# Kernel tuning notes

Measured on AMD Instinct MI355X. Metric: run time of the kernel, lower is better.

The kernel has to match this reference:

```python
import jax, jax.numpy as jnp
import numpy as np
import math

D_MODEL, NHEAD, FACTOR = 1024, 16, 5
EPS = 1e-5


def layer_norm(x, g, b):
    m = jnp.mean(x, -1, keepdims=True)
    v = jnp.mean((x - m) ** 2, -1, keepdims=True)
    return (x - m) / jnp.sqrt(v + EPS) * g + b


def prob_attention(q, k, v, sample_key):
    # Informer ProbSparse causal self-attention. q,k,v: [B,H,L,E]
    B, H, L_Q, E = q.shape
    L_K = k.shape[2]
    U_part = min(FACTOR * int(np.ceil(np.log(L_K))), L_K)  # sampled keys per query
    u = min(FACTOR * int(np.ceil(np.log(L_Q))), L_Q)        # top queries kept
    idx = jax.random.randint(sample_key, (L_Q, U_part), 0, L_K)
    K_sample = k[:, :, idx, :]                               # [B,H,L_Q,U,E]
    QK_sample = jnp.einsum('bhle,bhlue->bhlu', q, K_sample)
    M = QK_sample.max(-1) - QK_sample.sum(-1) / L_K          # sparsity measure
    _, M_top = jax.lax.top_k(M, u)                           # [B,H,u] query indices
    Q_red = jnp.take_along_axis(q, M_top[..., None], axis=2) # [B,H,u,E]
    scores = jnp.einsum('bhue,bhse->bhus', Q_red, k) / math.sqrt(E)
    causal = jnp.arange(L_K)[None, None, None, :] > M_top[..., None]
    scores = jnp.where(causal, -1e9, scores)
    attn = jax.nn.softmax(scores, -1)
    upd = jnp.einsum('bhus,bhsd->bhud', attn, v)             # [B,H,u,E]
    ctx = jnp.cumsum(v, axis=2)                              # causal initial context
    b_i = jnp.arange(B)[:, None, None]
    h_i = jnp.arange(H)[None, :, None]
    return ctx.at[b_i, h_i, M_top].set(upd)


def full_attention(q, k, v):
    # q: [B,L,H,E], k,v: [B,S,H,E]; unmasked cross attention
    E = q.shape[-1]
    scores = jnp.einsum('blhe,bshe->bhls', q, k) / math.sqrt(E)
    A = jax.nn.softmax(scores, -1)
    return jnp.einsum('bhls,bshd->blhd', A, v)


def split_heads(t, B, L):
    return t.reshape(B, L, NHEAD, -1)


def decoder_layer(x, memory, sWq, sbq, sWk, sbk, sWv, sbv, sWo, sbo,
                  cWq, cbq, cWk, cbk, cWv, cbv, cWo, cbo,
                  W1, b1, W2, b2, g1, be1, g2, be2, g3, be3):
    B, L, D = x.shape
    S = memory.shape[1]
    # --- ProbSparse self-attention ---
    q = split_heads(x @ sWq + sbq, B, L).transpose(0, 2, 1, 3)
    k = split_heads(x @ sWk + sbk, B, L).transpose(0, 2, 1, 3)
    v = split_heads(x @ sWv + sbv, B, L).transpose(0, 2, 1, 3)
    ctx = prob_attention(q, k, v, jax.random.key(42))
    sa = ctx.transpose(0, 2, 1, 3).reshape(B, L, D) @ sWo + sbo
    x = layer_norm(x + sa, g1, be1)
    # --- full cross-attention ---
    q = split_heads(x @ cWq + cbq, B, L)
    k = split_heads(memory @ cWk + cbk, B, S)
    v = split_heads(memory @ cWv + cbv, B, S)
    ca = full_attention(q, k, v).reshape(B, L, D) @ cWo + cbo
    x = layer_norm(x + ca, g2, be2)
    # --- conv1d(k=1) FFN == pointwise MLP ---
    y = jax.nn.relu(x @ W1 + b1)
    y = y @ W2 + b2
    return layer_norm(x + y, g3, be3)


def setup_inputs() -> dict:
    key = jax.random.key(0)
    ks = jax.random.split(key, 32)
    D, F = D_MODEL, 4 * D_MODEL
    w = lambda k, sh: (jax.random.normal(k, sh, jnp.float32) * 0.02)
    inp = {
        'x': jax.random.normal(ks[0], (2, 2048, D), jnp.float32),
        'memory': jax.random.normal(ks[1], (2, 2048, D), jnp.float32),
    }
    names = ['sWq', 'sWk', 'sWv', 'sWo', 'cWq', 'cWk', 'cWv', 'cWo']
    for i, n in enumerate(names):
        inp[n] = w(ks[2 + i], (D, D))
        inp[n.replace('W', 'b')] = jnp.zeros((D,), jnp.float32)
    inp['W1'] = w(ks[10], (D, F)); inp['b1'] = jnp.zeros((F,), jnp.float32)
    inp['W2'] = w(ks[11], (F, D)); inp['b2'] = jnp.zeros((D,), jnp.float32)
    for i, n in enumerate(['1', '2', '3']):
        inp['g' + n] = jnp.ones((D,), jnp.float32)
        inp['be' + n] = jnp.zeros((D,), jnp.float32)
    return inp


def reference(x, memory, sWq, sbq, sWk, sbk, sWv, sbv, sWo, sbo,
              cWq, cbq, cWk, cbk, cWv, cbv, cWo, cbo,
              W1, b1, W2, b2, g1, be1, g2, be2, g3, be3):
    return decoder_layer(x, memory, sWq, sbq, sWk, sbk, sWv, sbv, sWo, sbo,
                         cWq, cbq, cWk, cbk, cWv, cbv, cWo, cbo,
                         W1, b1, W2, b2, g1, be1, g2, be2, g3, be3)
```

## Files before the change

### kernel.cpp

```cpp
#include <hip/hip_runtime.h>

static constexpr int BATCH  = 2;
static constexpr int SEQ    = 2048;
static constexpr int DMODEL = 1024;
static constexpr int NHEADS = 16;
static constexpr int EHEAD  = 64;
static constexpr int DFF    = 4096;
static constexpr int NTOP   = 40;

typedef unsigned short u16;
typedef __bf16 bf16x8_t __attribute__((ext_vector_type(8)));
typedef u16    u16x8_t  __attribute__((ext_vector_type(8)));
typedef u16    u16x4_t  __attribute__((ext_vector_type(4)));
typedef float  f32x4_t  __attribute__((ext_vector_type(4)));

static constexpr float QSCALE = 0.125f * 1.44269504088896f;
static constexpr float FIXM   = 12.0f;

static __device__ __forceinline__ u16 f2b(float f) {
  unsigned u = __builtin_bit_cast(unsigned, f);
  unsigned r = u + 0x7FFFu + ((u >> 16) & 1u);
  return (u16)(r >> 16);
}
static __device__ __forceinline__ u16 f2bf(float f) {
  __bf16 h = (__bf16)f;
  return __builtin_bit_cast(u16, h);
}
static __device__ __forceinline__ float b2f(u16 h) {
  unsigned u = ((unsigned)h) << 16;
  return __builtin_bit_cast(float, u);
}
static __device__ __forceinline__ f32x4_t mfma_bf16(u16x8_t a, u16x8_t b, f32x4_t c) {
  return __builtin_amdgcn_mfma_f32_16x16x32_bf16(
      __builtin_bit_cast(bf16x8_t, a), __builtin_bit_cast(bf16x8_t, b), c, 0, 0, 0);
}

#define GLD16(gsrc, ldst)                                                        \
  __builtin_amdgcn_global_load_lds(                                             \
      (const __attribute__((address_space(1))) void*)(gsrc),                    \
      (__attribute__((address_space(3))) void*)(ldst), 16, 0, 0)

static __device__ __forceinline__ void tf2x32(unsigned k0, unsigned k1,
                                              unsigned x0, unsigned x1,
                                              unsigned& o0, unsigned& o1) {
  unsigned ks2 = 0x1BD11BDAu ^ k0 ^ k1;
  x0 += k0; x1 += k1;
#define TFR(r) { x0 += x1; x1 = (x1 << r) | (x1 >> (32 - r)); x1 ^= x0; }
  TFR(13) TFR(15) TFR(26) TFR(6)  x0 += k1;  x1 += ks2 + 1u;
  TFR(17) TFR(29) TFR(16) TFR(24) x0 += ks2; x1 += k0 + 2u;
  TFR(13) TFR(15) TFR(26) TFR(6)  x0 += k0;  x1 += k1 + 3u;
  TFR(17) TFR(29) TFR(16) TFR(24) x0 += k1;  x1 += ks2 + 4u;
  TFR(13) TFR(15) TFR(26) TFR(6)  x0 += ks2; x1 += k0 + 5u;
#undef TFR
  o0 = x0; o1 = x1;
}

__global__ __launch_bounds__(256)
void prep_misc(const float* __restrict__ x, u16* __restrict__ xh,
               u16* __restrict__ xl, const float* __restrict__ mem,
               u16* __restrict__ memb, int* __restrict__ idx,
               const float* __restrict__ sbq, const float* __restrict__ sbk,
               float* __restrict__ biasqk, const float* __restrict__ cbk,
               const float* __restrict__ cbv, float* __restrict__ cbkv) {
  int blk = blockIdx.x, tid = threadIdx.x;
  if (blk < 4096) {
    int i = blk * 256 + tid;
    f32x4_t v = *(const f32x4_t*)(x + (size_t)i * 4);
    u16x4_t h, l;
#pragma unroll
    for (int d = 0; d < 4; ++d) {
      u16 hh = f2b(v[d]); h[d] = hh; l[d] = f2b(v[d] - b2f(hh));
    }
    *(u16x4_t*)(xh + (size_t)i * 4) = h;
    *(u16x4_t*)(xl + (size_t)i * 4) = l;
  } else if (blk < 8192) {
    int i = (blk - 4096) * 256 + tid;
    f32x4_t v = *(const f32x4_t*)(mem + (size_t)i * 4);
    u16x4_t o;
    o[0] = f2b(v[0]); o[1] = f2b(v[1]); o[2] = f2b(v[2]); o[3] = f2b(v[3]);
    *(u16x4_t*)(memb + (size_t)i * 4) = o;
  } else if (blk < 8512) {
    int i = (blk - 8192) * 256 + tid;
    unsigned c0, c1, o0, o1;
    tf2x32(0u, 42u, 0u, 1u, c0, c1);
    tf2x32(c0, c1, 0u, (unsigned)i, o0, o1);
    idx[i] = (int)((o0 ^ o1) & 2047u);
  } else {
    int i = (blk - 8512) * 256 + tid;
    if (i < 1024) biasqk[i] = sbq[i];
    else if (i < 2048) biasqk[i] = sbk[i - 1024];
    else if (i < 3072) cbkv[i - 2048] = cbk[i - 2048];
    else cbkv[i - 2048] = cbv[i - 3072];
  }
}

struct PrepW {
  const float* s2[2]; u16* dh2[2]; u16* dl2[2];
  const float* s6[6]; u16* d6[6];
  const float* W1; u16* W1T; const float* W2; u16* W2T;
};
__global__ __launch_bounds__(256)
void prep_weights(PrepW p) {
  __shared__ float t[64][65];
  int j = blockIdx.x;
  int c = threadIdx.x & 63, r4 = threadIdx.x >> 6;
  const float* in; u16* oh; u16* ol = nullptr;
  int K, N, k0, n0;
  if (j < 512) {
    int m = j >> 8, jj = j & 255;
    in = p.s2[m]; oh = p.dh2[m]; ol = p.dl2[m];
    K = 1024; N = 1024; n0 = (jj & 15) * 64; k0 = (jj >> 4) * 64;
  } else if (j < 2048) {
    int m = (j - 512) >> 8, jj = (j - 512) & 255;
    in = p.s6[m]; oh = p.d6[m];
    K = 1024; N = 1024; n0 = (jj & 15) * 64; k0 = (jj >> 4) * 64;
  } else if (j < 3072) {
    int jj = j - 2048;
    in = p.W1; oh = p.W1T;
    K = 1024; N = 4096; n0 = (jj & 63) * 64; k0 = (jj >> 6) * 64;
  } else {
    int jj = j - 3072;
    in = p.W2; oh = p.W2T;
    K = 4096; N = 1024; n0 = (jj & 15) * 64; k0 = (jj >> 4) * 64;
  }
#pragma unroll
  for (int i = 0; i < 16; ++i) {
    int r = r4 * 16 + i;
    t[r][c] = in[(size_t)(k0 + r) * N + n0 + c];
  }
  __syncthreads();
#pragma unroll
  for (int i = 0; i < 16; ++i) {
    int r = r4 * 16 + i;
    float f = t[c][r];
    u16 h = f2b(f);
    oh[(size_t)(n0 + r) * K + k0 + c] = h;
    if (ol) ol[(size_t)(n0 + r) * K + k0 + c] = f2b(f - b2f(h));
  }
}

template<int NF>
__global__ __launch_bounds__(256)
void gemm_bf(const u16* __restrict__ A, const u16* __restrict__ Bt,
             const float* __restrict__ bias, float* __restrict__ Cf,
             u16* __restrict__ Cb, int M, int N, int K, int relu) {
  __shared__ __align__(16) u16 sA[2][128 * 32];
  __shared__ __align__(16) u16 sB[2][NF * 32 * 32];
  const int tid = threadIdx.x;
  const int wave = tid >> 6, lane = tid & 63;
  const int m0 = blockIdx.x * 128, n0 = blockIdx.y * (NF * 32);
  const int wr = (wave >> 1) * 64, wc = (wave & 1) * (NF * 16);
  const int lr = lane & 15, kg = lane >> 4;
  const int wv = __builtin_amdgcn_readfirstlane(wave);

  int rowA[2], c8A[2];
#pragma unroll
  for (int rep = 0; rep < 2; ++rep) {
    int P = (rep * 256 + tid) << 4;
    int L = P ^ (((P >> 7) & 3) << 4);
    rowA[rep] = L >> 6; c8A[rep] = (L >> 4) & 3;
  }
  int rowB[NF / 2], c8B[NF / 2];
#pragma unroll
  for (int rep = 0; rep < NF / 2; ++rep) {
    int P = (rep * 256 + tid) << 4;
    int L = P ^ (((P >> 7) & 3) << 4);
    rowB[rep] = L >> 6; c8B[rep] = (L >> 4) & 3;
  }

  f32x4_t acc[4][NF];
#pragma unroll
  for (int i = 0; i < 4; ++i)
#pragma unroll
    for (int j = 0; j < NF; ++j) acc[i][j] = f32x4_t{0.f, 0.f, 0.f, 0.f};

  auto STAGE = [&](int buf, int k0) {
#pragma unroll
    for (int rep = 0; rep < 2; ++rep)
      GLD16(A + (size_t)(m0 + rowA[rep]) * K + k0 + c8A[rep] * 8,
            &sA[buf][(rep * 256 + wv * 64) * 8]);
#pragma unroll
    for (int rep = 0; rep < NF / 2; ++rep)
      GLD16(Bt + (size_t)(n0 + rowB[rep]) * K + k0 + c8B[rep] * 8,
            &sB[buf][(rep * 256 + wv * 64) * 8]);
  };

  const int nk = K >> 5;
  STAGE(0, 0);
  __syncthreads();
  for (int t = 0; t < nk; ++t) {
    const int cur = t & 1;
    if (t + 1 < nk) STAGE(cur ^ 1, (t + 1) << 5);
    u16x8_t a8[4], b8[NF];
#pragma unroll
    for (int mi = 0; mi < 4; ++mi) {
      int La = (wr + mi * 16 + lr) * 64 + kg * 16;
      a8[mi] = *(const u16x8_t*)((const char*)sA[cur] + (La ^ (((La >> 7) & 3) << 4)));
    }
#pragma unroll
    for (int ni = 0; ni < NF; ++ni) {
      int Lb = (wc + ni * 16 + lr) * 64 + kg * 16;
      b8[ni] = *(const u16x8_t*)((const char*)sB[cur] + (Lb ^ (((Lb >> 7) & 3) << 4)));
    }
#pragma unroll
    for (int mi = 0; mi < 4; ++mi)
#pragma unroll
      for (int ni = 0; ni < NF; ++ni)
        acc[mi][ni] = mfma_bf16(a8[mi], b8[ni], acc[mi][ni]);
    __syncthreads();
  }
#pragma unroll
  for (int ni = 0; ni < NF; ++ni) {
    int col = n0 + wc + ni * 16 + lr;
    float bc = bias[col];
#pragma unroll
    for (int mi = 0; mi < 4; ++mi)
#pragma unroll
      for (int r = 0; r < 4; ++r) {
        int row = m0 + wr + mi * 16 + kg * 4 + r;
        float vv = acc[mi][ni][r] + bc;
        if (relu) vv = fmaxf(vv, 0.f);
        if (Cf) Cf[(size_t)row * N + col] = vv;
        if (Cb) Cb[(size_t)row * N + col] = f2b(vv);
      }
  }
}

template<int NF>
__global__ __launch_bounds__(256)
void gemm_ks(const u16* __restrict__ A, const u16* __restrict__ Bt,
             const float* __restrict__ bias, float* __restrict__ C0,
             float* __restrict__ C1, int M, int N, int K) {
  __shared__ __align__(16) u16 sA[2][128 * 32];
  __shared__ __align__(16) u16 sB[2][NF * 32 * 32];
  const int tid = threadIdx.x;
  const int wave = tid >> 6, lane = tid & 63;
  const int m0 = blockIdx.x * 128, n0 = blockIdx.y * (NF * 32);
  const int zz = blockIdx.z;
  const int Kh = K >> 1;
  const u16* Ab = A + (size_t)zz * Kh;
  const u16* Bb = Bt + (size_t)zz * Kh;
  float* Cf = zz ? C1 : C0;
  const int wr = (wave >> 1) * 64, wc = (wave & 1) * (NF * 16);
  const int lr = lane & 15, kg = lane >> 4;
  const int wv = __builtin_amdgcn_readfirstlane(wave);

  int rowA[2], c8A[2];
#pragma unroll
  for (int rep = 0; rep < 2; ++rep) {
    int P = (rep * 256 + tid) << 4;
    int L = P ^ (((P >> 7) & 3) << 4);
    rowA[rep] = L >> 6; c8A[rep] = (L >> 4) & 3;
  }
  int rowB[NF / 2], c8B[NF / 2];
#pragma unroll
  for (int rep = 0; rep < NF / 2; ++rep) {
    int P = (rep * 256 + tid) << 4;
    int L = P ^ (((P >> 7) & 3) << 4);
    rowB[rep] = L >> 6; c8B[rep] = (L >> 4) & 3;
  }

  f32x4_t acc[4][NF];
#pragma unroll
  for (int i = 0; i < 4; ++i)
#pragma unroll
    for (int j = 0; j < NF; ++j) acc[i][j] = f32x4_t{0.f, 0.f, 0.f, 0.f};

  auto STAGE = [&](int buf, int k0) {
#pragma unroll
    for (int rep = 0; rep < 2; ++rep)
      GLD16(Ab + (size_t)(m0 + rowA[rep]) * K + k0 + c8A[rep] * 8,
            &sA[buf][(rep * 256 + wv * 64) * 8]);
#pragma unroll
    for (int rep = 0; rep < NF / 2; ++rep)
      GLD16(Bb + (size_t)(n0 + rowB[rep]) * K + k0 + c8B[rep] * 8,
            &sB[buf][(rep * 256 + wv * 64) * 8]);
  };

  const int nk = Kh >> 5;
  STAGE(0, 0);
  __syncthreads();
  for (int t = 0; t < nk; ++t) {
    const int cur = t & 1;
    if (t + 1 < nk) STAGE(cur ^ 1, (t + 1) << 5);
    u16x8_t a8[4], b8[NF];
#pragma unroll
    for (int mi = 0; mi < 4; ++mi) {
      int La = (wr + mi * 16 + lr) * 64 + kg * 16;
      a8[mi] = *(const u16x8_t*)((const char*)sA[cur] + (La ^ (((La >> 7) & 3) << 4)));
    }
#pragma unroll
    for (int ni = 0; ni < NF; ++ni) {
      int Lb = (wc + ni * 16 + lr) * 64 + kg * 16;
      b8[ni] = *(const u16x8_t*)((const char*)sB[cur] + (Lb ^ (((Lb >> 7) & 3) << 4)));
    }
#pragma unroll
    for (int mi = 0; mi < 4; ++mi)
#pragma unroll
      for (int ni = 0; ni < NF; ++ni)
        acc[mi][ni] = mfma_bf16(a8[mi], b8[ni], acc[mi][ni]);
    __syncthreads();
  }
#pragma unroll
  for (int ni = 0; ni < NF; ++ni) {
    int col = n0 + wc + ni * 16 + lr;
    float bc = (zz == 0) ? bias[col] : 0.f;
#pragma unroll
    for (int mi = 0; mi < 4; ++mi)
#pragma unroll
      for (int r = 0; r < 4; ++r) {
        int row = m0 + wr + mi * 16 + kg * 4 + r;
        Cf[(size_t)row * N + col] = acc[mi][ni][r] + bc;
      }
  }
}

template<int NF>
__global__ __launch_bounds__(256)
void gemm4_bf(const u16* __restrict__ Ah, const u16* __restrict__ Al,
              const u16* __restrict__ Bh, const u16* __restrict__ Bl,
              const float* __restrict__ bias, float* __restrict__ Cf,
              int M, int N, int K) {
  __shared__ __align__(16) u16 sAh[2][128 * 32];
  __shared__ __align__(16) u16 sAl[2][128 * 32];
  __shared__ __align__(16) u16 sBh[2][NF * 32 * 32];
  __shared__ __align__(16) u16 sBl[2][NF * 32 * 32];
  const int tid = threadIdx.x;
  const int wave = tid >> 6, lane = tid & 63;
  const int m0 = blockIdx.x * 128, n0 = blockIdx.y * (NF * 32);
  const int wr = (wave >> 1) * 64, wc = (wave & 1) * (NF * 16);
  const int lr = lane & 15, kg = lane >> 4;
  const int wv = __builtin_amdgcn_readfirstlane(wave);

  int rowA[2], c8A[2];
#pragma unroll
  for (int rep = 0; rep < 2; ++rep) {
    int P = (rep * 256 + tid) << 4;
    int L = P ^ (((P >> 7) & 3) << 4);
    rowA[rep] = L >> 6; c8A[rep] = (L >> 4) & 3;
  }
  int rowB[NF / 2], c8B[NF / 2];
#pragma unroll
  for (int rep = 0; rep < NF / 2; ++rep) {
    int P = (rep * 256 + tid) << 4;
    int L = P ^ (((P >> 7) & 3) << 4);
    rowB[rep] = L >> 6; c8B[rep] = (L >> 4) & 3;
  }

  f32x4_t acc[4][NF];
#pragma unroll
  for (int i = 0; i < 4; ++i)
#pragma unroll
    for (int j = 0; j < NF; ++j) acc[i][j] = f32x4_t{0.f, 0.f, 0.f, 0.f};

  auto STAGE = [&](int buf, int k0) {
#pragma unroll
    for (int rep = 0; rep < 2; ++rep) {
      GLD16(Ah + (size_t)(m0 + rowA[rep]) * K + k0 + c8A[rep] * 8,
            &sAh[buf][(rep * 256 + wv * 64) * 8]);
      GLD16(Al + (size_t)(m0 + rowA[rep]) * K + k0 + c8A[rep] * 8,
            &sAl[buf][(rep * 256 + wv * 64) * 8]);
    }
#pragma unroll
    for (int rep = 0; rep < NF / 2; ++rep) {
      GLD16(Bh + (size_t)(n0 + rowB[rep]) * K + k0 + c8B[rep] * 8,
            &sBh[buf][(rep * 256 + wv * 64) * 8]);
      GLD16(Bl + (size_t)(n0 + rowB[rep]) * K + k0 + c8B[rep] * 8,
            &sBl[buf][(rep * 256 + wv * 64) * 8]);
    }
  };

  const int nk = K >> 5;
  STAGE(0, 0);
  __syncthreads();
  for (int t = 0; t < nk; ++t) {
    const int cur = t & 1;
    if (t + 1 < nk) STAGE(cur ^ 1, (t + 1) << 5);
    u16x8_t ah[4], al[4], bh[NF], bl[NF];
#pragma unroll
    for (int mi = 0; mi < 4; ++mi) {
      int La = (wr + mi * 16 + lr) * 64 + kg * 16;
      int off = La ^ (((La >> 7) & 3) << 4);
      ah[mi] = *(const u16x8_t*)((const char*)sAh[cur] + off);
      al[mi] = *(const u16x8_t*)((const char*)sAl[cur] + off);
    }
#pragma unroll
    for (int ni = 0; ni < NF; ++ni) {
      int Lb = (wc + ni * 16 + lr) * 64 + kg * 16;
      int off = Lb ^ (((Lb >> 7) & 3) << 4);
      bh[ni] = *(const u16x8_t*)((const char*)sBh[cur] + off);
      bl[ni] = *(const u16x8_t*)((const char*)sBl[cur] + off);
    }
#pragma unroll
    for (int mi = 0; mi < 4; ++mi)
#pragma unroll
      for (int ni = 0; ni < NF; ++ni) {
        acc[mi][ni] = mfma_bf16(ah[mi], bh[ni], acc[mi][ni]);
        acc[mi][ni] = mfma_bf16(ah[mi], bl[ni], acc[mi][ni]);
        acc[mi][ni] = mfma_bf16(al[mi], bh[ni], acc[mi][ni]);
      }
    __syncthreads();
  }
#pragma unroll
  for (int ni = 0; ni < NF; ++ni) {
    int col = n0 + wc + ni * 16 + lr;
    float bc = bias[col];
#pragma unroll
    for (int mi = 0; mi < 4; ++mi)
#pragma unroll
      for (int r = 0; r < 4; ++r) {
        int row = m0 + wr + mi * 16 + kg * 4 + r;
        Cf[(size_t)row * N + col] = acc[mi][ni][r] + bc;
      }
  }
}

__global__ __launch_bounds__(256)
void probM_kernel(const float* __restrict__ qk, const int* __restrict__ idx,
                  float* __restrict__ Mv) {
  int blk = blockIdx.x;
  int xcd = blk & 7, j = blk >> 3;
  int b = xcd >> 2;
  int part = (xcd & 3) * 128 + j;
  int l = part * 4 + (threadIdx.x >> 6);
  int lane = threadIdx.x & 63;
  const float* qrow = qk + ((size_t)b * SEQ + l) * 2048 + lane * 16;
  f32x4_t qv0 = *(const f32x4_t*)(qrow);
  f32x4_t qv1 = *(const f32x4_t*)(qrow + 4);
  f32x4_t qv2 = *(const f32x4_t*)(qrow + 8);
  f32x4_t qv3 = *(const f32x4_t*)(qrow + 12);
  const int* ip = idx + l * NTOP;
  const float* kbase = qk + (size_t)b * SEQ * 2048 + 1024 + lane * 16;
  float mmax = -3.0e38f, msum = 0.f;
  for (int pass = 0; pass < 4; ++pass) {
    int lo = pass << 9;
#pragma unroll 4
    for (int u = 0; u < NTOP; ++u) {
      int ki = ip[u];
      if ((unsigned)(ki - lo) < 512u) {
        const float* kr = kbase + (size_t)ki * 2048;
        f32x4_t k0 = *(const f32x4_t*)(kr);
        f32x4_t k1 = *(const f32x4_t*)(kr + 4);
        f32x4_t k2 = *(const f32x4_t*)(kr + 8);
        f32x4_t k3 = *(const f32x4_t*)(kr + 12);
        float p = qv0[0] * k0[0] + qv0[1] * k0[1] + qv0[2] * k0[2] + qv0[3] * k0[3]
                + qv1[0] * k1[0] + qv1[1] * k1[1] + qv1[2] * k1[2] + qv1[3] * k1[3]
                + qv2[0] * k2[0] + qv2[1] * k2[1] + qv2[2] * k2[2] + qv2[3] * k2[3]
                + qv3[0] * k3[0] + qv3[1] * k3[1] + qv3[2] * k3[2] + qv3[3] * k3[3];
        p += __shfl_xor(p, 1);
        p += __shfl_xor(p, 2);
        mmax = fmaxf(mmax, p);
        msum += p;
      }
    }
  }
  if ((lane & 3) == 0) {
    int hh = lane >> 2;
    Mv[((size_t)b * NHEADS + hh) * SEQ + l] = mmax - msum * (1.f / 2048.f);
  }
}

__global__ __launch_bounds__(256)
void topk_kernel(const float* __restrict__ Mv, int* __restrict__ Mtop) {
  int bh = blockIdx.x;
  int tid = threadIdx.x;
  int lane = tid & 63, wv = tid >> 6;
  float v8[8];
#pragma unroll
  for (int j = 0; j < 8; ++j) v8[j] = Mv[bh * 2048 + j * 256 + tid];
  __shared__ float wrv[4];
  __shared__ int wri[4];
  __shared__ int winner;
  for (int it = 0; it < NTOP; ++it) {
    float best = v8[0];
    int bj = 0;
#pragma unroll
    for (int j = 1; j < 8; ++j)
      if (v8[j] > best) { best = v8[j]; bj = j; }
    int bi = bj * 256 + tid;
#pragma unroll
    for (int m = 1; m < 64; m <<= 1) {
      float ov = __shfl_xor(best, m);
      int oi = __shfl_xor(bi, m);
      if (ov > best || (ov == best && oi < bi)) { best = ov; bi = oi; }
    }
    if (lane == 0) { wrv[wv] = best; wri[wv] = bi; }
    __syncthreads();
    if (tid == 0) {
      float bv = wrv[0]; int bbi = wri[0];
#pragma unroll
      for (int t = 1; t < 4; ++t)
        if (wrv[t] > bv || (wrv[t] == bv && wri[t] < bbi)) { bv = wrv[t]; bbi = wri[t]; }
      Mtop[bh * NTOP + it] = bbi;
      winner = bbi;
    }
    __syncthreads();
    int w = winner;
#pragma unroll
    for (int j = 0; j < 8; ++j)
      if ((w >> 8) == j && (w & 255) == tid) v8[j] = -3.4e38f;
  }
}

__global__ __launch_bounds__(256)
void kvpack_self(const float* __restrict__ qk, const u16* __restrict__ vbf,
                 u16* __restrict__ kpack, u16* __restrict__ vpack) {
  int bh = blockIdx.x, ch = blockIdx.y;
  int b = bh >> 4, hh = bh & 15;
  int tid = threadIdx.x;
  __shared__ u16 vt[64][80];
#pragma unroll
  for (int rep = 0; rep < 2; ++rep) {
    int u = rep * 256 + tid;
    int key = u >> 3, c = u & 7;
    const float* ksrc = qk + ((size_t)(b * SEQ + ch * 64 + key)) * 2048 + 1024 + hh * 64 + c * 8;
    f32x4_t k0 = *(const f32x4_t*)ksrc;
    f32x4_t k1 = *(const f32x4_t*)(ksrc + 4);
    u16x8_t d;
    d[0] = f2bf(k0[0]); d[1] = f2bf(k0[1]); d[2] = f2bf(k0[2]); d[3] = f2bf(k0[3]);
    d[4] = f2bf(k1[0]); d[5] = f2bf(k1[1]); d[6] = f2bf(k1[2]); d[7] = f2bf(k1[3]);
    int slot = (key & 3) | (((key >> 3) & 1) << 2);
    *(u16x8_t*)(kpack + ((size_t)bh * SEQ + ch * 64 + key) * 64 + ((c ^ slot) * 8)) = d;
    u16x8_t dv = *(const u16x8_t*)(vbf + ((size_t)(b * SEQ + ch * 64 + key)) * 1024 + hh * 64 + c * 8);
    *(u16x8_t*)(&vt[key][c * 8]) = dv;
  }
  __syncthreads();
#pragma unroll
  for (int rep = 0; rep < 2; ++rep) {
    int u = rep * 256 + tid;
    int e = u >> 3, c = u & 7;
    int kb = (c ^ (e & 7)) * 8;
    u16x8_t d;
#pragma unroll
    for (int j = 0; j < 8; ++j) d[j] = vt[kb + j][e];
    *(u16x8_t*)(vpack + (((size_t)bh * 32 + ch) * 64 + e) * 64 + c * 8) = d;
  }
}

__global__ __launch_bounds__(256)
void probAttn_kernel(const float* __restrict__ qk, const u16* __restrict__ kpack,
                     const u16* __restrict__ vpack, const int* __restrict__ Mtop,
                     float* __restrict__ Opart, float* __restrict__ ml) {
  const int bh = blockIdx.x, b = bh >> 4, hh = bh & 15;
  const int split = blockIdx.y;
  const int tid = threadIdx.x, wave = tid >> 6, lane = tid & 63;
  const int lr = lane & 15, kg = lane >> 4;
  const int wv = __builtin_amdgcn_readfirstlane(wave);
  __shared__ __align__(16) u16 Qs[48 * 64];
  __shared__ __align__(16) u16 Kt[2][64 * 64];
  __shared__ __align__(16) u16 Vt[2][64 * 64];

#pragma unroll
  for (int rep = 0; rep < 3; ++rep) {
    int j = tid + 256 * rep;
    int row = j >> 4, c4 = j & 15;
    int qi = Mtop[bh * NTOP + (row < NTOP ? row : NTOP - 1)];
    f32x4_t v4 = *(const f32x4_t*)(qk + ((size_t)b * SEQ + qi) * 2048 + hh * EHEAD + c4 * 4);
    u16x4_t b4;
    b4[0] = f2bf(v4[0] * QSCALE); b4[1] = f2bf(v4[1] * QSCALE);
    b4[2] = f2bf(v4[2] * QSCALE); b4[3] = f2bf(v4[3] * QSCALE);
    *(u16x4_t*)((char*)Qs + ((row * 128 + c4 * 8) ^ ((row & 7) << 4))) = b4;
  }

  const int qtile = (wave < 3) ? wave : 2;
  const int qrow_g = qtile * 16 + lr;
  const int iq = (qrow_g < NTOP) ? Mtop[bh * NTOP + qrow_g] : -1;

  int koffs[2][4], voffs[2][4], kbase16[4];
#pragma unroll
  for (int t4 = 0; t4 < 4; ++t4) {
    int arow = ((t4 >> 1) << 5) + ((lr >> 2) << 3) + ((t4 & 1) << 2) + (lr & 3);
    int slot = (arow & 3) | (((arow >> 3) & 1) << 2);
#pragma unroll
    for (int ks = 0; ks < 2; ++ks)
      koffs[ks][t4] = ((arow << 7) + (ks << 6) + (kg << 4)) ^ (slot << 4);
    kbase16[t4] = ((t4 >> 1) << 5) + (kg << 3) + ((t4 & 1) << 2);
  }
#pragma unroll
  for (int ne = 0; ne < 4; ++ne) {
    int e = ne * 16 + lr;
#pragma unroll
    for (int ks2 = 0; ks2 < 2; ++ks2)
      voffs[ks2][ne] = ((e << 7) + (ks2 << 6) + (kg << 4)) ^ ((e & 7) << 4);
  }
  const int maskbase = split * 256 - iq;

  const char* kgl = (const char*)kpack + (size_t)bh * SEQ * 128 + (size_t)split * 4 * 8192;
  const char* vgl = (const char*)vpack + (size_t)bh * 32 * 8192 + (size_t)split * 4 * 8192;
  auto STAGE = [&](int buf, int t) {
    GLD16(kgl + (size_t)t * 8192 + wv * 2048 + lane * 16, (char*)Kt[buf] + wv * 2048);
    GLD16(kgl + (size_t)t * 8192 + wv * 2048 + 1024 + lane * 16, (char*)Kt[buf] + wv * 2048 + 1024);
    GLD16(vgl + (size_t)t * 8192 + wv * 2048 + lane * 16, (char*)Vt[buf] + wv * 2048);
    GLD16(vgl + (size_t)t * 8192 + wv * 2048 + 1024 + lane * 16, (char*)Vt[buf] + wv * 2048 + 1024);
  };

  STAGE(0, 0);
  __syncthreads();

  u16x8_t bq[2];
  {
    int qrow = qtile * 16 + lr;
#pragma unroll
    for (int ks = 0; ks < 2; ++ks)
      bq[ks] = *(u16x8_t*)((char*)Qs + ((qrow * 128 + ks * 64 + kg * 16) ^ ((qrow & 7) << 4)));
  }

  f32x4_t oacc[4];
#pragma unroll
  for (int i = 0; i < 4; ++i) oacc[i] = f32x4_t{0.f, 0.f, 0.f, 0.f};
  float lsum = 0.f;

  for (int t = 0; t < 4; ++t) {
    const int cur = t & 1;
    if (t + 1 < 4) STAGE(cur ^ 1, t + 1);
    const char* kb = (const char*)Kt + cur * 8192;
    const char* vb = (const char*)Vt + cur * 8192;
    f32x4_t s[4];
#pragma unroll
    for (int i = 0; i < 4; ++i) s[i] = f32x4_t{-FIXM, -FIXM, -FIXM, -FIXM};
#pragma unroll
    for (int ks = 0; ks < 2; ++ks)
#pragma unroll
      for (int t4 = 0; t4 < 4; ++t4) {
        u16x8_t ak = *(const u16x8_t*)(kb + koffs[ks][t4]);
        s[t4] = mfma_bf16(ak, bq[ks], s[t4]);
      }
    const int mb = t * 64 + maskbase;
#pragma unroll
    for (int t4 = 0; t4 < 4; ++t4)
#pragma unroll
      for (int r = 0; r < 4; ++r)
        if (mb + kbase16[t4] + r > 0) s[t4][r] = -1e9f;
#pragma unroll
    for (int t4 = 0; t4 < 4; ++t4)
#pragma unroll
      for (int r = 0; r < 4; ++r) {
        float p = exp2f(s[t4][r]);
        s[t4][r] = p; lsum += p;
      }
#pragma unroll
    for (int ks2 = 0; ks2 < 2; ++ks2) {
      u16x8_t pa;
#pragma unroll
      for (int j = 0; j < 4; ++j) {
        pa[j] = f2bf(s[2 * ks2][j]);
        pa[4 + j] = f2bf(s[2 * ks2 + 1][j]);
      }
#pragma unroll
      for (int ne = 0; ne < 4; ++ne) {
        u16x8_t bv = *(const u16x8_t*)(vb + voffs[ks2][ne]);
        oacc[ne] = mfma_bf16(pa, bv, oacc[ne]);
      }
    }
    __syncthreads();
  }

  lsum += __shfl_xor(lsum, 16);
  lsum += __shfl_xor(lsum, 32);

  if (wave < 3) {
    float* ob = Opart + (((size_t)(bh * 8 + split)) * 48 + qtile * 16) * 64;
#pragma unroll
    for (int ne = 0; ne < 4; ++ne)
#pragma unroll
      for (int r = 0; r < 4; ++r)
        ob[(size_t)(kg * 4 + r) * 64 + ne * 16 + lr] = oacc[ne][r];
    if (kg == 0)
      ml[((size_t)(bh * 8 + split)) * 48 + qtile * 16 + lr] = lsum;
  }
}

__global__ __launch_bounds__(64)
void probCombine_kernel(const float* __restrict__ Opart, const float* __restrict__ ml,
                        const int* __restrict__ Mtop, u16* __restrict__ ctxb) {
  int bh = blockIdx.x / NTOP, q = blockIdx.x % NTOP;
  int e = threadIdx.x;
  int b = bh >> 4, hh = bh & 15;
  float lstar = 0.f, acc = 0.f;
#pragma unroll
  for (int s = 0; s < 8; ++s) {
    lstar += ml[((size_t)(bh * 8 + s)) * 48 + q];
    acc += Opart[(((size_t)(bh * 8 + s)) * 48 + q) * 64 + e];
  }
  int row = Mtop[bh * NTOP + q];
  ctxb[((size_t)b * SEQ + row) * DMODEL + hh * EHEAD + e] = f2bf(acc / lstar);
}

__global__ __launch_bounds__(64)
void scanA_kernel(const u16* __restrict__ v, float* __restrict__ csum) {
  int bh = blockIdx.x, ch = blockIdx.y;
  int b = bh >> 4, hh = bh & 15, e = threadIdx.x;
  size_t base = ((size_t)b * SEQ + ch * 128) * DMODEL + hh * EHEAD + e;
  float run = 0.f;
  for (int i = 0; i < 128; ++i) run += b2f(v[base + (size_t)i * DMODEL]);
  csum[(bh * 16 + ch) * 64 + e] = run;
}
__global__ __launch_bounds__(64)
void scanB_kernel(const u16* __restrict__ v, const float* __restrict__ csum,
                  u16* __restrict__ ctxb) {
  int bh = blockIdx.x, ch = blockIdx.y;
  int b = bh >> 4, hh = bh & 15, e = threadIdx.x;
  float run = 0.f;
  for (int cc = 0; cc < ch; ++cc) run += csum[(bh * 16 + cc) * 64 + e];
  size_t base = ((size_t)b * SEQ + ch * 128) * DMODEL + hh * EHEAD + e;
  for (int i = 0; i < 128; ++i) {
    run += b2f(v[base + (size_t)i * DMODEL]);
    ctxb[base + (size_t)i * DMODEL] = f2bf(run);
  }
}

__global__ __launch_bounds__(256)
void kvpack_kernel(const u16* __restrict__ kv, u16* __restrict__ kpack,
                   u16* __restrict__ vpack) {
  int bh = blockIdx.x, ch = blockIdx.y;
  int b = bh >> 4, hh = bh & 15;
  int tid = threadIdx.x;
  __shared__ u16 vt[64][80];
#pragma unroll
  for (int rep = 0; rep < 2; ++rep) {
    int u = rep * 256 + tid;
    int key = u >> 3, c = u & 7;
    u16x8_t d = *(const u16x8_t*)(kv + ((size_t)(b * SEQ + ch * 64 + key)) * 2048 + hh * 64 + c * 8);
    int slot = (key & 3) | (((key >> 3) & 1) << 2);
    *(u16x8_t*)(kpack + ((size_t)bh * SEQ + ch * 64 + key) * 64 + ((c ^ slot) * 8)) = d;
    u16x8_t dv = *(const u16x8_t*)(kv + ((size_t)(b * SEQ + ch * 64 + key)) * 2048 + 1024 + hh * 64 + c * 8);
    *(u16x8_t*)(&vt[key][c * 8]) = dv;
  }
  __syncthreads();
#pragma unroll
  for (int rep = 0; rep < 2; ++rep) {
    int u = rep * 256 + tid;
    int e = u >> 3, c = u & 7;
    int kb = (c ^ (e & 7)) * 8;
    u16x8_t d;
#pragma unroll
    for (int j = 0; j < 8; ++j) d[j] = vt[kb + j][e];
    *(u16x8_t*)(vpack + (((size_t)bh * 32 + ch) * 64 + e) * 64 + c * 8) = d;
  }
}

__global__ __launch_bounds__(512)
void cross_attn_kernel(const float* __restrict__ q2, const u16* __restrict__ kpack,
                       const u16* __restrict__ vpack, u16* __restrict__ cab) {
  const int bh = blockIdx.x, b = bh >> 4, hh = bh & 15;
  const int qt0 = blockIdx.y * 128;
  const int tid = threadIdx.x, wave = tid >> 6, lane = tid & 63;
  const int lr = lane & 15, kg = lane >> 4;
  const int wv = __builtin_amdgcn_readfirstlane(wave);
  __shared__ __align__(16) u16 Qs[128 * 64];
  __shared__ __align__(16) u16 Kt[2][64 * 64];
  __shared__ __align__(16) u16 Vt[2][64 * 64];

#pragma unroll
  for (int i = 0; i < 4; ++i) {
    int j = tid + 512 * i;
    int row = j >> 4, c4 = j & 15;
    f32x4_t v4 = *(const f32x4_t*)(q2 + ((size_t)b * SEQ + qt0 + row) * DMODEL + hh * EHEAD + c4 * 4);
    u16x4_t b4;
    b4[0] = f2bf(v4[0] * QSCALE); b4[1] = f2bf(v4[1] * QSCALE);
    b4[2] = f2bf(v4[2] * QSCALE); b4[3] = f2bf(v4[3] * QSCALE);
    *(u16x4_t*)((char*)Qs + ((row * 128 + c4 * 8) ^ ((row & 7) << 4))) = b4;
  }

  int koffs[2][4], voffs[2][4];
#pragma unroll
  for (int t4 = 0; t4 < 4; ++t4) {
    int arow = ((t4 >> 1) << 5) + ((lr >> 2) << 3) + ((t4 & 1) << 2) + (lr & 3);
    int slot = (arow & 3) | (((arow >> 3) & 1) << 2);
#pragma unroll
    for (int ks = 0; ks < 2; ++ks)
      koffs[ks][t4] = ((arow << 7) + (ks << 6) + (kg << 4)) ^ (slot << 4);
  }
#pragma unroll
  for (int ne = 0; ne < 4; ++ne) {
    int e = ne * 16 + lr;
#pragma unroll
    for (int ks2 = 0; ks2 < 2; ++ks2)
      voffs[ks2][ne] = ((e << 7) + (ks2 << 6) + (kg << 4)) ^ ((e & 7) << 4);
  }

  const char* kgl = (const char*)kpack + (size_t)bh * SEQ * 128;
  const char* vgl = (const char*)vpack + (size_t)bh * 32 * 8192;
  auto STAGE = [&](int buf, int t) {
    GLD16(kgl + (size_t)t * 8192 + wv * 1024 + lane * 16, (char*)Kt[buf] + wv * 1024);
    GLD16(vgl + (size_t)t * 8192 + wv * 1024 + lane * 16, (char*)Vt[buf] + wv * 1024);
  };

  STAGE(0, 0);
  __syncthreads();

  u16x8_t bq[2];
  {
    int qrow = wave * 16 + lr;
#pragma unroll
    for (int ks = 0; ks < 2; ++ks)
      bq[ks] = *(u16x8_t*)((char*)Qs + ((qrow * 128 + ks * 64 + kg * 16) ^ ((qrow & 7) << 4)));
  }

  f32x4_t oacc[4];
#pragma unroll
  for (int i = 0; i < 4; ++i) oacc[i] = f32x4_t{0.f, 0.f, 0.f, 0.f};
  float lsum = 0.f;

  for (int t = 0; t < 32; ++t) {
    const int cur = t & 1;
    if (t + 1 < 32) STAGE(cur ^ 1, t + 1);
    const char* kb = (const char*)Kt + cur * 8192;
    const char* vb = (const char*)Vt + cur * 8192;
    f32x4_t s[4];
#pragma unroll
    for (int i = 0; i < 4; ++i) s[i] = f32x4_t{-FIXM, -FIXM, -FIXM, -FIXM};
#pragma unroll
    for (int ks = 0; ks < 2; ++ks)
#pragma unroll
      for (int t4 = 0; t4 < 4; ++t4) {
        u16x8_t ak = *(const u16x8_t*)(kb + koffs[ks][t4]);
        s[t4] = mfma_bf16(ak, bq[ks], s[t4]);
      }
#pragma unroll
    for (int t4 = 0; t4 < 4; ++t4)
#pragma unroll
      for (int r = 0; r < 4; ++r) {
        float p = exp2f(s[t4][r]);
        s[t4][r] = p; lsum += p;
      }
#pragma unroll
    for (int ks2 = 0; ks2 < 2; ++ks2) {
      u16x8_t pa;
#pragma unroll
      for (int j = 0; j < 4; ++j) {
        pa[j] = f2bf(s[2 * ks2][j]);
        pa[4 + j] = f2bf(s[2 * ks2 + 1][j]);
      }
#pragma unroll
      for (int ne = 0; ne < 4; ++ne) {
        u16x8_t bv = *(const u16x8_t*)(vb + voffs[ks2][ne]);
        oacc[ne] = mfma_bf16(pa, bv, oacc[ne]);
      }
    }
    __syncthreads();
  }

  lsum += __shfl_xor(lsum, 16);
  lsum += __shfl_xor(lsum, 32);
  float inv4[4];
#pragma unroll
  for (int r = 0; r < 4; ++r) inv4[r] = 1.0f / __shfl(lsum, kg * 4 + r);
#pragma unroll
  for (int ne = 0; ne < 4; ++ne)
#pragma unroll
    for (int r = 0; r < 4; ++r) {
      int row = qt0 + wave * 16 + kg * 4 + r;
      int col = hh * EHEAD + ne * 16 + lr;
      cab[((size_t)b * SEQ + row) * DMODEL + col] = f2bf(oacc[ne][r] * inv4[r]);
    }
}

__global__ __launch_bounds__(256)
void ln_kernel(const float* __restrict__ x, const float* __restrict__ r,
               const float* __restrict__ g, const float* __restrict__ be,
               float* __restrict__ outf, u16* __restrict__ outb) {
  int row = blockIdx.x, tid = threadIdx.x;
  size_t base = (size_t)row * DMODEL;
  float v[4];
  float s = 0.f, sq = 0.f;
#pragma unroll
  for (int i = 0; i < 4; ++i) {
    int c = tid + i * 256;
    float t = x[base + c] + r[base + c];
    v[i] = t; s += t; sq += t * t;
  }
  __shared__ float rs[256], rq[256];
  rs[tid] = s; rq[tid] = sq;
  __syncthreads();
  for (int st = 128; st > 0; st >>= 1) {
    if (tid < st) { rs[tid] += rs[tid + st]; rq[tid] += rq[tid + st]; }
    __syncthreads();
  }
  float mean = rs[0] * (1.f / DMODEL);
  float var = rq[0] * (1.f / DMODEL) - mean * mean;
  float rstd = rsqrtf(var + 1e-5f);
#pragma unroll
  for (int i = 0; i < 4; ++i) {
    int c = tid + i * 256;
    float o = (v[i] - mean) * rstd * g[c] + be[c];
    if (outf) outf[base + c] = o;
    if (outb) outb[base + c] = f2bf(o);
  }
}

__global__ __launch_bounds__(256)
void ln3_kernel(const float* __restrict__ x, const float* __restrict__ r0,
                const float* __restrict__ r1, const float* __restrict__ g,
                const float* __restrict__ be, float* __restrict__ outf,
                u16* __restrict__ outb) {
  int row = blockIdx.x, tid = threadIdx.x;
  size_t base = (size_t)row * DMODEL;
  float v[4];
  float s = 0.f, sq = 0.f;
#pragma unroll
  for (int i = 0; i < 4; ++i) {
    int c = tid + i * 256;
    float t = x[base + c] + r0[base + c] + r1[base + c];
    v[i] = t; s += t; sq += t * t;
  }
  __shared__ float rs[256], rq[256];
  rs[tid] = s; rq[tid] = sq;
  __syncthreads();
  for (int st = 128; st > 0; st >>= 1) {
    if (tid < st) { rs[tid] += rs[tid + st]; rq[tid] += rq[tid + st]; }
    __syncthreads();
  }
  float mean = rs[0] * (1.f / DMODEL);
  float var = rq[0] * (1.f / DMODEL) - mean * mean;
  float rstd = rsqrtf(var + 1e-5f);
#pragma unroll
  for (int i = 0; i < 4; ++i) {
    int c = tid + i * 256;
    float o = (v[i] - mean) * rstd * g[c] + be[c];
    if (outf) outf[base + c] = o;
    if (outb) outb[base + c] = f2bf(o);
  }
}

static inline void gemm(const u16* A, const u16* Bt, const float* bias, float* Cf,
                        u16* Cb, int M, int N, int K, int relu, hipStream_t s,
                        int big = 0) {
  if (big)
    gemm_bf<4><<<dim3(M / 128, N / 128), 256, 0, s>>>(A, Bt, bias, Cf, Cb, M, N, K, relu);
  else
    gemm_bf<2><<<dim3(M / 128, N / 64), 256, 0, s>>>(A, Bt, bias, Cf, Cb, M, N, K, relu);
}
static inline void gemmks(const u16* A, const u16* Bt, const float* bias, float* C0,
                          float* C1, int M, int N, int K, hipStream_t s) {
  gemm_ks<4><<<dim3(M / 128, N / 128, 2), 256, 0, s>>>(A, Bt, bias, C0, C1, M, N, K);
}
static inline void gemm4(const u16* Ah, const u16* Al, const u16* Bh, const u16* Bl,
                         const float* bias, float* Cf, int M, int N, int K, hipStream_t s) {
  gemm4_bf<4><<<dim3(M / 128, N / 128), 256, 0, s>>>(Ah, Al, Bh, Bl, bias, Cf, M, N, K);
}

extern "C" void kernel_launch(void* const* d_in, const int* in_sizes, int n_in,
                              void* d_out, int out_size, void* d_ws, size_t ws_size,
                              hipStream_t stream) {
  const float* x   = (const float*)d_in[0];
  const float* mem = (const float*)d_in[1];
  const float* sWq = (const float*)d_in[2];  const float* sbq = (const float*)d_in[3];
  const float* sWk = (const float*)d_in[4];  const float* sbk = (const float*)d_in[5];
  const float* sWv = (const float*)d_in[6];  const float* sbv = (const float*)d_in[7];
  const float* sWo = (const float*)d_in[8];  const float* sbo = (const float*)d_in[9];
  const float* cWq = (const float*)d_in[10]; const float* cbq = (const float*)d_in[11];
  const float* cWk = (const float*)d_in[12]; const float* cbk = (const float*)d_in[13];
  const float* cWv = (const float*)d_in[14]; const float* cbv = (const float*)d_in[15];
  const float* cWo = (const float*)d_in[16]; const float* cbo = (const float*)d_in[17];
  const float* W1  = (const float*)d_in[18]; const float* b1  = (const float*)d_in[19];
  const float* W2  = (const float*)d_in[20]; const float* b2  = (const float*)d_in[21];
  const float* g1  = (const float*)d_in[22]; const float* be1 = (const float*)d_in[23];
  const float* g2  = (const float*)d_in[24]; const float* be2 = (const float*)d_in[25];
  const float* g3  = (const float*)d_in[26]; const float* be3 = (const float*)d_in[27];
  float* outp = (float*)d_out;
  char* ws = (char*)d_ws;
  const size_t MB = 1ull << 20;

  int*   idx    = (int*)(ws);
  float* Mv     = (float*)(ws + 0x60000);
  int*   Mtop   = (int*)(ws + 0xA0000);
  float* biasqk = (float*)(ws + 0x120000);
  float* cbkv   = (float*)(ws + 0x122000);
  float* csum   = (float*)(ws + 0x130000);

  u16* WqkhT = (u16*)(ws + 2 * MB);
  u16* WqklT = (u16*)(ws + 6 * MB);
  u16* sWvT  = (u16*)(ws + 10 * MB);
  u16* sWoT  = (u16*)(ws + 12 * MB);
  u16* cWqT  = (u16*)(ws + 14 * MB);
  u16* cWkvT = (u16*)(ws + 16 * MB);
  u16* cWoT  = (u16*)(ws + 20 * MB);
  u16* W1T   = (u16*)(ws + 22 * MB);
  u16* W2T   = (u16*)(ws + 30 * MB);

  u16* xh   = (u16*)(ws + 38 * MB);
  u16* xl   = (u16*)(ws + 46 * MB);
  u16* memb = (u16*)(ws + 54 * MB);

  float* qk    = (float*)(ws + 62 * MB);
  u16*   vbf   = (u16*)(ws + 94 * MB);
  u16*   kpks  = (u16*)(ws + 102 * MB);
  u16*   vpks  = (u16*)(ws + 46 * MB);
  float* Opart = (float*)(ws + 110 * MB);
  float* mlbuf = (float*)(ws + 113 * MB);
  u16*   ctxb  = (u16*)(ws + 78 * MB);
  float* sa    = (float*)(ws + 94 * MB);
  float* x1    = (float*)(ws + 62 * MB);
  u16*   x1b   = (u16*)(ws + 78 * MB);
  float* q2    = (float*)(ws + 94 * MB);
  u16*   kv2b  = (u16*)(ws + 38 * MB);
  u16*   kpk   = (u16*)(ws + 54 * MB);
  u16*   vpk   = (u16*)(ws + 110 * MB);
  u16*   cab   = (u16*)(ws + 38 * MB);
  float* ca0   = (float*)(ws + 94 * MB);
  float* ca1   = (float*)(ws + 2 * MB);
  float* x2    = (float*)(ws + 38 * MB);
  u16*   x2b   = (u16*)(ws + 54 * MB);
  u16*   hbb   = (u16*)(ws + 62 * MB);
  float* yb0   = (float*)(ws + 94 * MB);
  float* yb1   = (float*)(ws + 2 * MB);

  const int MROWS = BATCH * SEQ;

  prep_misc<<<8528, 256, 0, stream>>>(x, xh, xl, mem, memb, idx,
                                      sbq, sbk, biasqk, cbk, cbv, cbkv);
  {
    PrepW p;
    p.s2[0] = sWq; p.dh2[0] = WqkhT;               p.dl2[0] = WqklT;
    p.s2[1] = sWk; p.dh2[1] = WqkhT + 1024 * 1024; p.dl2[1] = WqklT + 1024 * 1024;
    p.s6[0] = sWv; p.d6[0] = sWvT;
    p.s6[1] = sWo; p.d6[1] = sWoT;
    p.s6[2] = cWq; p.d6[2] = cWqT;
    p.s6[3] = cWk; p.d6[3] = cWkvT;
    p.s6[4] = cWv; p.d6[4] = cWkvT + 1024 * 1024;
    p.s6[5] = cWo; p.d6[5] = cWoT;
    p.W1 = W1; p.W1T = W1T; p.W2 = W2; p.W2T = W2T;
    prep_weights<<<4096, 256, 0, stream>>>(p);
  }

  gemm4(xh, xl, WqkhT, WqklT, biasqk, qk, MROWS, 2048, DMODEL, stream);
  gemm(xh, sWvT, sbv, nullptr, vbf, MROWS, DMODEL, DMODEL, 0, stream);
  probM_kernel<<<BATCH * SEQ / 4, 256, 0, stream>>>(qk, idx, Mv);
  topk_kernel<<<BATCH * NHEADS, 256, 0, stream>>>(Mv, Mtop);
  kvpack_self<<<dim3(BATCH * NHEADS, SEQ / 64), 256, 0, stream>>>(qk, vbf, kpks, vpks);
  probAttn_kernel<<<dim3(BATCH * NHEADS, 8), 256, 0, stream>>>(qk, kpks, vpks, Mtop, Opart, mlbuf);
  scanA_kernel<<<dim3(BATCH * NHEADS, 16), 64, 0, stream>>>(vbf, csum);
  scanB_kernel<<<dim3(BATCH * NHEADS, 16), 64, 0, stream>>>(vbf, csum, ctxb);
  probCombine_kernel<<<BATCH * NHEADS * NTOP, 64, 0, stream>>>(Opart, mlbuf, Mtop, ctxb);
  gemm(ctxb, sWoT, sbo, sa, nullptr, MROWS, DMODEL, DMODEL, 0, stream);
  ln_kernel<<<MROWS, 256, 0, stream>>>(x, sa, g1, be1, x1, x1b);

  gemm(x1b, cWqT, cbq, q2, nullptr, MROWS, DMODEL, DMODEL, 0, stream);
  gemm(memb, cWkvT, cbkv, nullptr, kv2b, MROWS, 2048, DMODEL, 0, stream, 1);
  kvpack_kernel<<<dim3(BATCH * NHEADS, SEQ / 64), 256, 0, stream>>>(kv2b, kpk, vpk);
  cross_attn_kernel<<<dim3(BATCH * NHEADS, SEQ / 128), 512, 0, stream>>>(q2, kpk, vpk, cab);
  gemmks(cab, cWoT, cbo, ca0, ca1, MROWS, DMODEL, DMODEL, stream);
  ln3_kernel<<<MROWS, 256, 0, stream>>>(x1, ca0, ca1, g2, be2, x2, x2b);

  gemm(x2b, W1T, b1, nullptr, hbb, MROWS, DFF, DMODEL, 1, stream, 1);
  gemmks(hbb, W2T, b2, yb0, yb1, MROWS, DMODEL, DFF, stream);
  ln3_kernel<<<MROWS, 256, 0, stream>>>(x2, yb0, yb1, g3, be3, outp, nullptr);
}
```

Baseline: 526.9 us.

## Split cross-attention over key halves and add a combine kernel

```diff
diff --git a/kernel.cpp b/kernel.cpp
--- a/kernel.cpp
+++ b/kernel.cpp
@@ -741,9 +741,11 @@
 
 __global__ __launch_bounds__(512)
 void cross_attn_kernel(const float* __restrict__ q2, const u16* __restrict__ kpack,
-                       const u16* __restrict__ vpack, u16* __restrict__ cab) {
+                       const u16* __restrict__ vpack, u16* __restrict__ Opb,
+                       float* __restrict__ lsb) {
   const int bh = blockIdx.x, b = bh >> 4, hh = bh & 15;
   const int qt0 = blockIdx.y * 128;
+  const int split = blockIdx.z;
   const int tid = threadIdx.x, wave = tid >> 6, lane = tid & 63;
   const int lr = lane & 15, kg = lane >> 4;
   const int wv = __builtin_amdgcn_readfirstlane(wave);
@@ -779,8 +781,8 @@
       voffs[ks2][ne] = ((e << 7) + (ks2 << 6) + (kg << 4)) ^ ((e & 7) << 4);
   }
 
-  const char* kgl = (const char*)kpack + (size_t)bh * SEQ * 128;
-  const char* vgl = (const char*)vpack + (size_t)bh * 32 * 8192;
+  const char* kgl = (const char*)kpack + (size_t)bh * SEQ * 128 + (size_t)split * 1024 * 128;
+  const char* vgl = (const char*)vpack + (size_t)bh * 32 * 8192 + (size_t)split * 16 * 8192;
   auto STAGE = [&](int buf, int t) {
     GLD16(kgl + (size_t)t * 8192 + wv * 1024 + lane * 16, (char*)Kt[buf] + wv * 1024);
     GLD16(vgl + (size_t)t * 8192 + wv * 1024 + lane * 16, (char*)Vt[buf] + wv * 1024);
@@ -802,9 +804,9 @@
   for (int i = 0; i < 4; ++i) oacc[i] = f32x4_t{0.f, 0.f, 0.f, 0.f};
   float lsum = 0.f;
 
-  for (int t = 0; t < 32; ++t) {
+  for (int t = 0; t < 16; ++t) {
     const int cur = t & 1;
-    if (t + 1 < 32) STAGE(cur ^ 1, t + 1);
+    if (t + 1 < 16) STAGE(cur ^ 1, t + 1);
     const char* kb = (const char*)Kt + cur * 8192;
     const char* vb = (const char*)Vt + cur * 8192;
     f32x4_t s[4];
@@ -843,17 +845,36 @@
 
   lsum += __shfl_xor(lsum, 16);
   lsum += __shfl_xor(lsum, 32);
-  float inv4[4];
-#pragma unroll
-  for (int r = 0; r < 4; ++r) inv4[r] = 1.0f / __shfl(lsum, kg * 4 + r);
+
+  size_t gbase = ((size_t)split * 32 + bh) * 2048 + qt0;
 #pragma unroll
   for (int ne = 0; ne < 4; ++ne)
 #pragma unroll
     for (int r = 0; r < 4; ++r) {
-      int row = qt0 + wave * 16 + kg * 4 + r;
-      int col = hh * EHEAD + ne * 16 + lr;
-      cab[((size_t)b * SEQ + row) * DMODEL + col] = f2bf(oacc[ne][r] * inv4[r]);
-    }
+      int rowl = wave * 16 + kg * 4 + r;
+      Opb[(gbase + rowl) * 64 + ne * 16 + lr] = f2bf(oacc[ne][r]);
+    }
+  if (kg == 0)
+    lsb[gbase + wave * 16 + lr] = lsum;
+}
+
+__global__ __launch_bounds__(256)
+void caCombine_kernel(const u16* __restrict__ Opb, const float* __restrict__ lsb,
+                      u16* __restrict__ cab) {
+  int i = blockIdx.x * 256 + threadIdx.x;
+  int base = i * 4;
+  int g = base >> 6;
+  int col = base & 63;
+  u16x4_t p0 = *(const u16x4_t*)(Opb + (size_t)g * 64 + col);
+  u16x4_t p1 = *(const u16x4_t*)(Opb + ((size_t)65536 + g) * 64 + col);
+  float inv = 1.0f / (lsb[g] + lsb[65536 + g]);
+  int bh = g >> 11, row = g & 2047;
+  int b = bh >> 4, hh = bh & 15;
+  u16x4_t o;
+#pragma unroll
+  for (int d = 0; d < 4; ++d)
+    o[d] = f2bf((b2f(p0[d]) + b2f(p1[d])) * inv);
+  *(u16x4_t*)(cab + ((size_t)(b * 2048 + row)) * 1024 + hh * 64 + col) = o;
 }
 
 __global__ __launch_bounds__(256)
@@ -997,6 +1018,8 @@
   u16*   kv2b  = (u16*)(ws + 38 * MB);
   u16*   kpk   = (u16*)(ws + 54 * MB);
   u16*   vpk   = (u16*)(ws + 110 * MB);
+  u16*   Opb   = (u16*)(ws + 2 * MB);
+  float* lsb   = (float*)(ws + 18 * MB);
   u16*   cab   = (u16*)(ws + 38 * MB);
   float* ca0   = (float*)(ws + 94 * MB);
   float* ca1   = (float*)(ws + 2 * MB);
@@ -1039,7 +1062,8 @@
   gemm(x1b, cWqT, cbq, q2, nullptr, MROWS, DMODEL, DMODEL, 0, stream);
   gemm(memb, cWkvT, cbkv, nullptr, kv2b, MROWS, 2048, DMODEL, 0, stream, 1);
   kvpack_kernel<<<dim3(BATCH * NHEADS, SEQ / 64), 256, 0, stream>>>(kv2b, kpk, vpk);
-  cross_attn_kernel<<<dim3(BATCH * NHEADS, SEQ / 128), 512, 0, stream>>>(q2, kpk, vpk, cab);
+  cross_attn_kernel<<<dim3(BATCH * NHEADS, SEQ / 128, 2), 512, 0, stream>>>(q2, kpk, vpk, Opb, lsb);
+  caCombine_kernel<<<4096, 256, 0, stream>>>(Opb, lsb, cab);
   gemmks(cab, cWoT, cbo, ca0, ca1, MROWS, DMODEL, DMODEL, stream);
   ln3_kernel<<<MROWS, 256, 0, stream>>>(x1, ca0, ca1, g2, be2, x2, x2b);
 
```

Result: no change. 530.9 us (+0.8%).
